# Kernel tuning notes

Measured on AMD Instinct MI355X. Metric: run time of the kernel, lower is better.

Reference implementation:

```python
import jax, jax.numpy as jnp
import numpy as np

HEAD_DIM = 256
V_DIM = 256
HIDDEN = 1024
SCALE_BASE = 512
GAMMA = 0.96875
BATCH, SEQ = 4, 4096


def _dup_interleave(m):
    # (L, d/2) -> (L, d), duplicating each column consecutively
    return jnp.repeat(m, 2, axis=-1)


def _rotate_every_two(x):
    x1 = x[..., ::2]
    x2 = x[..., 1::2]
    return jnp.stack([-x2, x1], axis=-1).reshape(x.shape)


def _xpos(x, downscale=False):
    # x: (B, L, head_dim); offset=0 path of XPOS.forward
    B, L, Dh = x.shape
    half = Dh // 2
    scale_buf = (jnp.arange(0, Dh, 2, dtype=jnp.float32) + 0.4 * Dh) / (1.4 * Dh)  # (half,)
    pos = jnpp = jnp.arange(L, dtype=jnp.float32)
    scale = scale_buf[None, :] ** (pos / SCALE_BASE)[:, None]  # (L, half)
    inv_freq = 1.0 / (10000.0 ** (jnp.arange(half, dtype=jnp.float32) / half))
    sinusoid = pos[:, None] * inv_freq[None, :]  # (L, half)
    sin, cos = jnp.sin(sinusoid), jnp.cos(sinusoid)
    if downscale:
        scale = 1.0 / scale
    cos_s = _dup_interleave(cos * scale)  # (L, Dh)
    sin_s = _dup_interleave(sin * scale)
    return x * cos_s[None] + _rotate_every_two(x) * sin_s[None]


def _decay_matrix(L):
    n = jnp.arange(L)[:, None]
    m = jnp.arange(L)[None, :]
    mask = n >= m
    expo = jnp.where(mask, n - m, 0).astype(jnp.float32)
    return jnp.where(mask, GAMMA ** expo, 0.0)  # (L, L)


def setup_inputs() -> dict:
    key = jax.random.key(0)
    k1, k2, k3, k4 = jax.random.split(key, 4)
    X = jax.random.normal(k1, (BATCH, SEQ, HIDDEN), dtype=jnp.float32)
    W_Q = jax.random.normal(k2, (HIDDEN, HEAD_DIM), dtype=jnp.float32) / HIDDEN
    W_K = jax.random.normal(k3, (HIDDEN, HEAD_DIM), dtype=jnp.float32) / HIDDEN
    W_V = jax.random.normal(k4, (HIDDEN, V_DIM), dtype=jnp.float32) / HIDDEN
    return {"X": X, "W_Q": W_Q, "W_K": W_K, "W_V": W_V}


def reference(X, W_Q, W_K, W_V):
    L = X.shape[1]
    Q = _xpos(X @ W_Q)                      # (B, L, Dh)
    K = _xpos(X @ W_K, downscale=True)      # (B, L, Dh)
    V = X @ W_V                             # (B, L, Dv)
    D = _decay_matrix(L)                    # (L, L)
    ret = jnp.einsum('bqd,bkd->bqk', Q, K) * D[None]  # (B, L, L)
    return ret @ V                          # (B, L, Dv)
```

## Files before the change

### kernel.cpp

```cpp
#include <hip/hip_runtime.h>
#include <hip/hip_bf16.h>
#include <cstdint>
#include <cstddef>

#define L_SEQ 4096
#define BATCH_N 4
#define HID 1024
#define DH 256
#define LOG2_GAMMA (-0.045803689613124953f)

typedef __attribute__((ext_vector_type(8))) short short8;
typedef __attribute__((ext_vector_type(4))) float floatx4;

__device__ __forceinline__ unsigned short f2bf(float f) {
    union { float f; unsigned int u; } v; v.f = f;
    unsigned int r = (v.u + 0x7FFFu + ((v.u >> 16) & 1u)) >> 16;
    return (unsigned short)r;
}

__device__ __forceinline__ void async_copy16(const unsigned short* gsrc,
                                             unsigned short* lds) {
    __builtin_amdgcn_global_load_lds(
        (const __attribute__((address_space(1))) unsigned int*)gsrc,
        (__attribute__((address_space(3))) unsigned int*)lds, 16, 0, 0);
}

__global__ __launch_bounds__(256) void convert_x_kernel(
    const float* __restrict__ X, unsigned short* __restrict__ Xb)
{
    const int i = (blockIdx.x * 256 + threadIdx.x) * 4;
    const float4 v = *(const float4*)&X[i];
    ushort4 p;
    p.x = f2bf(v.x); p.y = f2bf(v.y); p.z = f2bf(v.z); p.w = f2bf(v.w);
    *(ushort4*)&Xb[i] = p;
}

__global__ __launch_bounds__(256) void xpos_table_kernel(
    float2* __restrict__ tabQ, float2* __restrict__ tabK)
{
    const int gid = blockIdx.x * 256 + threadIdx.x;
    const int i2  = gid >> 12;
    const int pos = gid & (L_SEQ - 1);
    const float e   = (float)pos * (1.0f / 512.0f);
    const float sb  = ((float)(2 * i2) + 102.4f) * (1.0f / 358.4f);
    const float scQ = exp2f(log2f(sb) * e);
    const float scK = 1.0f / scQ;
    const float invf = exp2f(-13.287712379549449f *
                             ((float)i2 * (1.0f / 128.0f)));
    float s, c;
    sincosf((float)pos * invf, &s, &c);
    tabQ[gid] = make_float2(c * scQ, s * scQ);
    tabK[gid] = make_float2(c * scK, s * scK);
}

__global__ __launch_bounds__(256) void transpose_w_kernel(
    const float* __restrict__ WQ, const float* __restrict__ WK,
    const float* __restrict__ WV, unsigned short* __restrict__ Wt)
{
    __shared__ float Ts[64][68];
    const int n0 = blockIdx.x * 64;
    const int k0 = blockIdx.y * 64;
    const int seg = n0 >> 8;
    const float* __restrict__ W = (seg == 0) ? WQ : (seg == 1) ? WK : WV;
    const int nl0 = n0 & 255;

    const int t  = threadIdx.x;
    const int r  = t >> 4;
    const int c4 = (t & 15) * 4;
    #pragma unroll
    for (int i = 0; i < 4; ++i) {
        const int kk = r + i * 16;
        const float4 v = *(const float4*)&W[(size_t)(k0 + kk) * DH + nl0 + c4];
        Ts[c4 + 0][kk] = v.x;
        Ts[c4 + 1][kk] = v.y;
        Ts[c4 + 2][kk] = v.z;
        Ts[c4 + 3][kk] = v.w;
    }
    __syncthreads();
    const int rn = t >> 3;
    const int c8 = (t & 7) * 8;
    #pragma unroll
    for (int i = 0; i < 2; ++i) {
        const int rr = rn + i * 32;
        ushort4 p0, p1;
        p0.x = f2bf(Ts[rr][c8 + 0]); p0.y = f2bf(Ts[rr][c8 + 1]);
        p0.z = f2bf(Ts[rr][c8 + 2]); p0.w = f2bf(Ts[rr][c8 + 3]);
        p1.x = f2bf(Ts[rr][c8 + 4]); p1.y = f2bf(Ts[rr][c8 + 5]);
        p1.z = f2bf(Ts[rr][c8 + 6]); p1.w = f2bf(Ts[rr][c8 + 7]);
        unsigned short* dst = &Wt[(size_t)(n0 + rr) * HID + k0 + c8];
        *(ushort4*)dst       = p0;
        *(ushort4*)(dst + 4) = p1;
    }
}

__global__ __launch_bounds__(256) void gemm_qkv_kernel(
    const unsigned short* __restrict__ Wt,
    const unsigned short* __restrict__ Xb,
    const float2* __restrict__ tabQ,
    const float2* __restrict__ tabK,
    unsigned short* __restrict__ Qo,
    unsigned short* __restrict__ Ko,
    unsigned short* __restrict__ VtG)
{
    __shared__ unsigned short Wa[3][128][32];
    __shared__ unsigned short Xs[3][128][32];

    const int dblk = blockIdx.x;
    const int xcd  = dblk & 7;
    const int sq   = dblk >> 3;
    const int by   = xcd * 16 + sq / 6;
    const int bx   = sq % 6;

    const int n0 = bx * 128;
    const int p0 = by * 128;
    const int t    = threadIdx.x;
    const int w    = t >> 6;
    const int lane = t & 63;
    const int quad = lane >> 4;
    const int l16  = lane & 15;
    const int wn   = (w & 1) * 64;
    const int wp   = (w >> 1) * 64;

    const int srow = w * 32 + (lane >> 2);
    const int scol = (lane & 3) * 8;

    floatx4 acc[4][4];
    #pragma unroll
    for (int i = 0; i < 4; ++i)
        #pragma unroll
        for (int j = 0; j < 4; ++j) acc[i][j] = (floatx4){0.f, 0.f, 0.f, 0.f};

    const int NT = HID / 32;

    auto stage = [&](int buf, int kt) {
        const int k0 = kt * 32;
        #pragma unroll
        for (int is = 0; is < 2; ++is) {
            const unsigned short* ga =
                &Wt[(size_t)(n0 + srow + is * 16) * HID + k0 + scol];
            const unsigned short* gb =
                &Xb[(size_t)(p0 + srow + is * 16) * HID + k0 + scol];
            async_copy16(ga, &Wa[buf][w * 32 + is * 16][0]);
            async_copy16(gb, &Xs[buf][w * 32 + is * 16][0]);
        }
    };

    stage(0, 0);
    stage(1, 1);

    for (int kt = 0; kt < NT; ++kt) {
        const int buf = kt % 3;
        if (kt + 1 < NT)
            asm volatile("s_waitcnt vmcnt(4)" ::: "memory");
        else
            asm volatile("s_waitcnt vmcnt(0)" ::: "memory");
        __builtin_amdgcn_s_barrier();

        if (kt + 2 < NT) stage((kt + 2) % 3, kt + 2);

        short8 af[4], bfv[4];
        #pragma unroll
        for (int nt = 0; nt < 4; ++nt)
            af[nt] = *(const short8*)&Wa[buf][wn + nt * 16 + l16][quad * 8];
        #pragma unroll
        for (int pt = 0; pt < 4; ++pt)
            bfv[pt] = *(const short8*)&Xs[buf][wp + pt * 16 + l16][quad * 8];
        #pragma unroll
        for (int nt = 0; nt < 4; ++nt)
            #pragma unroll
            for (int pt = 0; pt < 4; ++pt)
                acc[nt][pt] = __builtin_amdgcn_mfma_f32_16x16x32_bf16(
                    af[nt], bfv[pt], acc[nt][pt], 0, 0, 0);
    }

    const int seg = n0 >> 8;
    const float2* __restrict__ tab = (seg == 1) ? tabK : tabQ;
    #pragma unroll
    for (int nt = 0; nt < 4; ++nt) {
        const int nfeat = n0 + wn + nt * 16 + quad * 4;
        const int d0 = nfeat & 255;
        #pragma unroll
        for (int pt = 0; pt < 4; ++pt) {
            const int pg  = p0 + wp + pt * 16 + l16;
            const int b   = pg >> 12;
            const int pos = pg & (L_SEQ - 1);
            if (seg == 2) {
                #pragma unroll
                for (int g = 0; g < 4; ++g)
                    VtG[(((size_t)(b * 256 + d0 + g)) << 12) + pos] =
                        f2bf(acc[nt][pt][g]);
            } else {
                float res[4];
                #pragma unroll
                for (int h = 0; h < 4; h += 2) {
                    const int i2 = (d0 + h) >> 1;
                    const float2 tc = tab[(i2 << 12) + pos];
                    const float cs = tc.x, ss = tc.y;
                    const float xe = acc[nt][pt][h], xo = acc[nt][pt][h + 1];
                    res[h]     = xe * cs - xo * ss;
                    res[h + 1] = xo * cs + xe * ss;
                }
                ushort4 pk;
                pk.x = f2bf(res[0]); pk.y = f2bf(res[1]);
                pk.z = f2bf(res[2]); pk.w = f2bf(res[3]);
                unsigned short* orow =
                    ((seg == 0) ? Qo : Ko) + (size_t)pg * DH + d0;
                *(ushort4*)orow = pk;
            }
        }
    }
}

__global__ __launch_bounds__(256) void retention_kernel(
    const unsigned short* __restrict__ Q,
    const unsigned short* __restrict__ K,
    const unsigned short* __restrict__ VtG,
    float* __restrict__ O)
{
    __shared__ short Qs[64][264];
    __shared__ short Ks[32][264];
    __shared__ short Vt[256][40];
    __shared__ short Ss[64][40];

    const int dblk = blockIdx.x;
    const int xcd  = dblk & 7;
    const int sq   = dblk >> 3;
    const int qt   = xcd * 8 + (sq & 7);
    const int b    = (sq >> 3) & 3;
    const int z    = sq >> 5;

    const int t  = threadIdx.x;
    const int q0 = qt * 64;

    const int w    = t >> 6;
    const int lane = t & 63;
    const int quad = lane >> 4;
    const int l16  = lane & 15;
    const int w16  = w * 16;

    const size_t rbase = (size_t)b * L_SEQ * DH;
    const size_t vbase = ((size_t)b * DH) << 12;

    int kst = q0 - 512; if (kst < 0) kst = 0;
    const int half32 = ((q0 + 64 - kst) >> 6) << 5;
    const int kbeg = kst + (z ? half32 : 0);
    const int kfin = z ? (q0 + 64) : (kst + half32);

    {
        const unsigned short* src = Q + rbase + (size_t)q0 * DH;
        #pragma unroll
        for (int i = 0; i < 8; ++i) {
            const int row = i * 8 + (t >> 5);
            const int col = (t & 31) * 8;
            *(uint4*)&Qs[row][col] = *(const uint4*)&src[row * DH + col];
        }
    }

    floatx4 o[16];
    #pragma unroll
    for (int f = 0; f < 16; ++f) o[f] = (floatx4){0.f, 0.f, 0.f, 0.f};

    for (int k0 = kbeg; k0 < kfin; k0 += 32) {
        __syncthreads();
        {
            const unsigned short* src = K + rbase + (size_t)k0 * DH;
            #pragma unroll
            for (int i = 0; i < 4; ++i) {
                const int row = i * 8 + (t >> 5);
                const int col = (t & 31) * 8;
                *(uint4*)&Ks[row][col] = *(const uint4*)&src[row * DH + col];
            }
        }
        {
            const int c0   = t >> 2;
            const int koff = (t & 3) * 8;
            #pragma unroll
            for (int i = 0; i < 4; ++i) {
                const int c = c0 + 64 * i;
                *(uint4*)&Vt[c][koff] =
                    *(const uint4*)&VtG[vbase + ((size_t)c << 12) + k0 + koff];
            }
        }
        __syncthreads();

        floatx4 s00 = (floatx4){0.f, 0.f, 0.f, 0.f};
        floatx4 s01 = (floatx4){0.f, 0.f, 0.f, 0.f};
        floatx4 s10 = (floatx4){0.f, 0.f, 0.f, 0.f};
        floatx4 s11 = (floatx4){0.f, 0.f, 0.f, 0.f};
        #pragma unroll
        for (int dd = 0; dd < 4; ++dd) {
            const short8 aA  = *(const short8*)&Qs[w16 + l16][dd * 32 + quad * 8];
            const short8 aB  = *(const short8*)&Qs[w16 + l16][(dd + 4) * 32 + quad * 8];
            const short8 b0A = *(const short8*)&Ks[l16][dd * 32 + quad * 8];
            const short8 b1A = *(const short8*)&Ks[16 + l16][dd * 32 + quad * 8];
            const short8 b0B = *(const short8*)&Ks[l16][(dd + 4) * 32 + quad * 8];
            const short8 b1B = *(const short8*)&Ks[16 + l16][(dd + 4) * 32 + quad * 8];
            s00 = __builtin_amdgcn_mfma_f32_16x16x32_bf16(aA, b0A, s00, 0, 0, 0);
            s10 = __builtin_amdgcn_mfma_f32_16x16x32_bf16(aA, b1A, s10, 0, 0, 0);
            s01 = __builtin_amdgcn_mfma_f32_16x16x32_bf16(aB, b0B, s01, 0, 0, 0);
            s11 = __builtin_amdgcn_mfma_f32_16x16x32_bf16(aB, b1B, s11, 0, 0, 0);
        }
        #pragma unroll
        for (int nt = 0; nt < 2; ++nt) {
            const floatx4 sv = nt ? (s10 + s11) : (s00 + s01);
            const int kpos = k0 + nt * 16 + l16;
            #pragma unroll
            for (int g = 0; g < 4; ++g) {
                const int qpos = q0 + w16 + quad * 4 + g;
                const int dq = qpos - kpos;
                const float p = (dq >= 0) ? sv[g] * exp2f((float)dq * LOG2_GAMMA)
                                          : 0.0f;
                Ss[w16 + quad * 4 + g][nt * 16 + l16] = (short)f2bf(p);
            }
        }
        __syncthreads();

        {
            const short8 a = *(const short8*)&Ss[w16 + l16][quad * 8];
            #pragma unroll
            for (int f = 0; f < 16; ++f) {
                const short8 bfr = *(const short8*)&Vt[f * 16 + l16][quad * 8];
                o[f] = __builtin_amdgcn_mfma_f32_16x16x32_bf16(a, bfr, o[f], 0, 0, 0);
            }
        }
    }

    #pragma unroll
    for (int f = 0; f < 16; ++f) {
        #pragma unroll
        for (int g = 0; g < 4; ++g) {
            const int qpos = q0 + w16 + quad * 4 + g;
            atomicAdd(&O[rbase + (size_t)qpos * DH + f * 16 + l16], o[f][g]);
        }
    }
}

extern "C" void kernel_launch(void* const* d_in, const int* in_sizes, int n_in,
                              void* d_out, int out_size, void* d_ws, size_t ws_size,
                              hipStream_t stream)
{
    const float* X  = (const float*)d_in[0];
    const float* WQ = (const float*)d_in[1];
    const float* WK = (const float*)d_in[2];
    const float* WV = (const float*)d_in[3];
    float* out = (float*)d_out;

    const size_t per = (size_t)BATCH_N * L_SEQ * DH;
    unsigned short* Qw  = (unsigned short*)d_ws;
    unsigned short* Kw  = Qw + per;
    unsigned short* Vtw = Kw + per;
    unsigned short* Xbw = Vtw + per;
    unsigned short* Wtw = Xbw + (size_t)16384 * HID;
    float2* tabQ = (float2*)(Wtw + 786432);
    float2* tabK = tabQ + (size_t)128 * L_SEQ;

    hipMemsetAsync(out, 0, per * sizeof(float), stream);

    xpos_table_kernel<<<2048, 256, 0, stream>>>(tabQ, tabK);
    convert_x_kernel<<<16384, 256, 0, stream>>>(X, Xbw);
    transpose_w_kernel<<<dim3(12, 16), 256, 0, stream>>>(WQ, WK, WV, Wtw);

    gemm_qkv_kernel<<<768, 256, 0, stream>>>(Wtw, Xbw, tabQ, tabK, Qw, Kw, Vtw);

    retention_kernel<<<512, 256, 0, stream>>>(Qw, Kw, Vtw, out);
}
```

Baseline: 203.9 us.

## Keep Q fragments in registers and shuffle scores via bpermute instead of LDS

```diff
diff --git a/kernel.cpp b/kernel.cpp
--- a/kernel.cpp
+++ b/kernel.cpp
@@ -8,6 +8,7 @@
 #define HID 1024
 #define DH 256
 #define LOG2_GAMMA (-0.045803689613124953f)
+#define INV_GAMMA32 (2.7620582f)
 
 typedef __attribute__((ext_vector_type(8))) short short8;
 typedef __attribute__((ext_vector_type(4))) float floatx4;
@@ -217,10 +218,8 @@
     const unsigned short* __restrict__ VtG,
     float* __restrict__ O)
 {
-    __shared__ short Qs[64][264];
     __shared__ short Ks[32][264];
     __shared__ short Vt[256][40];
-    __shared__ short Ss[64][40];
 
     const int dblk = blockIdx.x;
     const int xcd  = dblk & 7;
@@ -246,19 +245,33 @@
     const int kbeg = kst + (z ? half32 : 0);
     const int kfin = z ? (q0 + 64) : (kst + half32);
 
+    short8 qf[8];
     {
-        const unsigned short* src = Q + rbase + (size_t)q0 * DH;
-        #pragma unroll
-        for (int i = 0; i < 8; ++i) {
-            const int row = i * 8 + (t >> 5);
-            const int col = (t & 31) * 8;
-            *(uint4*)&Qs[row][col] = *(const uint4*)&src[row * DH + col];
-        }
-    }
+        const unsigned short* qsrc = Q + rbase + (size_t)(q0 + w16 + l16) * DH;
+        #pragma unroll
+        for (int dd = 0; dd < 8; ++dd)
+            qf[dd] = *(const short8*)&qsrc[dd * 32 + quad * 8];
+    }
+
+    int   dint[8];
+    float dec[8];
+    #pragma unroll
+    for (int nt = 0; nt < 2; ++nt)
+        #pragma unroll
+        for (int g = 0; g < 4; ++g) {
+            const int idx = nt * 4 + g;
+            dint[idx] = (q0 + w16 + l16) - (kbeg + nt * 16 + quad * 4 + g);
+            dec[idx]  = exp2f((float)dint[idx] * LOG2_GAMMA);
+        }
 
     floatx4 o[16];
     #pragma unroll
     for (int f = 0; f < 16; ++f) o[f] = (floatx4){0.f, 0.f, 0.f, 0.f};
+
+    const int s0   = (quad & 1) * 2;
+    const int idxA = (s0 * 16 + l16) * 4;
+    const int idxB = idxA + 64;
+    const bool lo  = (quad < 2);
 
     for (int k0 = kbeg; k0 < kfin; k0 += 32) {
         __syncthreads();
@@ -283,45 +296,58 @@
         }
         __syncthreads();
 
-        floatx4 s00 = (floatx4){0.f, 0.f, 0.f, 0.f};
-        floatx4 s01 = (floatx4){0.f, 0.f, 0.f, 0.f};
-        floatx4 s10 = (floatx4){0.f, 0.f, 0.f, 0.f};
-        floatx4 s11 = (floatx4){0.f, 0.f, 0.f, 0.f};
+        floatx4 sA0 = (floatx4){0.f, 0.f, 0.f, 0.f};
+        floatx4 sA1 = (floatx4){0.f, 0.f, 0.f, 0.f};
+        floatx4 sB0 = (floatx4){0.f, 0.f, 0.f, 0.f};
+        floatx4 sB1 = (floatx4){0.f, 0.f, 0.f, 0.f};
         #pragma unroll
         for (int dd = 0; dd < 4; ++dd) {
-            const short8 aA  = *(const short8*)&Qs[w16 + l16][dd * 32 + quad * 8];
-            const short8 aB  = *(const short8*)&Qs[w16 + l16][(dd + 4) * 32 + quad * 8];
-            const short8 b0A = *(const short8*)&Ks[l16][dd * 32 + quad * 8];
-            const short8 b1A = *(const short8*)&Ks[16 + l16][dd * 32 + quad * 8];
-            const short8 b0B = *(const short8*)&Ks[l16][(dd + 4) * 32 + quad * 8];
-            const short8 b1B = *(const short8*)&Ks[16 + l16][(dd + 4) * 32 + quad * 8];
-            s00 = __builtin_amdgcn_mfma_f32_16x16x32_bf16(aA, b0A, s00, 0, 0, 0);
-            s10 = __builtin_amdgcn_mfma_f32_16x16x32_bf16(aA, b1A, s10, 0, 0, 0);
-            s01 = __builtin_amdgcn_mfma_f32_16x16x32_bf16(aB, b0B, s01, 0, 0, 0);
-            s11 = __builtin_amdgcn_mfma_f32_16x16x32_bf16(aB, b1B, s11, 0, 0, 0);
-        }
+            const short8 k0f = *(const short8*)&Ks[l16][dd * 32 + quad * 8];
+            const short8 k1f = *(const short8*)&Ks[16 + l16][dd * 32 + quad * 8];
+            const short8 k0g = *(const short8*)&Ks[l16][(dd + 4) * 32 + quad * 8];
+            const short8 k1g = *(const short8*)&Ks[16 + l16][(dd + 4) * 32 + quad * 8];
+            sA0 = __builtin_amdgcn_mfma_f32_16x16x32_bf16(k0f, qf[dd], sA0, 0, 0, 0);
+            sA1 = __builtin_amdgcn_mfma_f32_16x16x32_bf16(k1f, qf[dd], sA1, 0, 0, 0);
+            sB0 = __builtin_amdgcn_mfma_f32_16x16x32_bf16(k0g, qf[dd + 4], sB0, 0, 0, 0);
+            sB1 = __builtin_amdgcn_mfma_f32_16x16x32_bf16(k1g, qf[dd + 4], sB1, 0, 0, 0);
+        }
+        const floatx4 sv0 = sA0 + sB0;
+        const floatx4 sv1 = sA1 + sB1;
+
+        unsigned int pk01[2], pk23[2];
         #pragma unroll
         for (int nt = 0; nt < 2; ++nt) {
-            const floatx4 sv = nt ? (s10 + s11) : (s00 + s01);
-            const int kpos = k0 + nt * 16 + l16;
+            const floatx4 sv = nt ? sv1 : sv0;
+            float pv[4];
             #pragma unroll
             for (int g = 0; g < 4; ++g) {
-                const int qpos = q0 + w16 + quad * 4 + g;
-                const int dq = qpos - kpos;
-                const float p = (dq >= 0) ? sv[g] * exp2f((float)dq * LOG2_GAMMA)
-                                          : 0.0f;
-                Ss[w16 + quad * 4 + g][nt * 16 + l16] = (short)f2bf(p);
+                const int idx = nt * 4 + g;
+                pv[g] = (dint[idx] >= 0) ? sv[g] * dec[idx] : 0.0f;
             }
-        }
-        __syncthreads();
-
-        {
-            const short8 a = *(const short8*)&Ss[w16 + l16][quad * 8];
-            #pragma unroll
-            for (int f = 0; f < 16; ++f) {
-                const short8 bfr = *(const short8*)&Vt[f * 16 + l16][quad * 8];
-                o[f] = __builtin_amdgcn_mfma_f32_16x16x32_bf16(a, bfr, o[f], 0, 0, 0);
-            }
+            pk01[nt] = ((unsigned int)f2bf(pv[1]) << 16) | (unsigned int)f2bf(pv[0]);
+            pk23[nt] = ((unsigned int)f2bf(pv[3]) << 16) | (unsigned int)f2bf(pv[2]);
+        }
+        #pragma unroll
+        for (int i = 0; i < 8; ++i) { dint[i] -= 32; dec[i] *= INV_GAMMA32; }
+
+        const int a01_0 = __builtin_amdgcn_ds_bpermute(idxA, (int)pk01[0]);
+        const int a01_1 = __builtin_amdgcn_ds_bpermute(idxA, (int)pk01[1]);
+        const int a23_0 = __builtin_amdgcn_ds_bpermute(idxA, (int)pk23[0]);
+        const int a23_1 = __builtin_amdgcn_ds_bpermute(idxA, (int)pk23[1]);
+        const int b01_0 = __builtin_amdgcn_ds_bpermute(idxB, (int)pk01[0]);
+        const int b01_1 = __builtin_amdgcn_ds_bpermute(idxB, (int)pk01[1]);
+        const int b23_0 = __builtin_amdgcn_ds_bpermute(idxB, (int)pk23[0]);
+        const int b23_1 = __builtin_amdgcn_ds_bpermute(idxB, (int)pk23[1]);
+        union { int u[4]; short8 s8; } af;
+        af.u[0] = lo ? a01_0 : a01_1;
+        af.u[1] = lo ? a23_0 : a23_1;
+        af.u[2] = lo ? b01_0 : b01_1;
+        af.u[3] = lo ? b23_0 : b23_1;
+
+        #pragma unroll
+        for (int f = 0; f < 16; ++f) {
+            const short8 bfr = *(const short8*)&Vt[f * 16 + l16][quad * 8];
+            o[f] = __builtin_amdgcn_mfma_f32_16x16x32_bf16(af.s8, bfr, o[f], 0, 0, 0);
         }
     }
 
```

Result: no change. 203.0 us (-0.4%).
